# Performance work log

Measured on AMD Instinct MI355X. Metric: run time of the kernel, lower is better.

Reference implementation:

```python
import jax, jax.numpy as jnp
import numpy as np

B, PIX_H, PIX_W = 64, 14, 14
ENC_D, DEC_D, ATT_D, EMB_D = 2048, 512, 512, 512
VOCAB, MAX_LEN = 10000, 52  # 51 decode steps


def setup_inputs() -> dict:
    key = jax.random.key(0)
    ks = jax.random.split(key, 24)
    s = 0.02
    inp = {
        'encoder_out': jax.random.normal(ks[0], (B, PIX_H, PIX_W, ENC_D), jnp.float32),
        'encoded_captions': jax.random.randint(ks[1], (B, MAX_LEN), 0, VOCAB),
        'caption_lengths': jnp.sort(jax.random.randint(ks[2], (B,), 2, MAX_LEN + 1))[::-1].at[0].set(MAX_LEN),
        # embedding (uniform -0.1..0.1 as in init_weights)
        'emb': jax.random.uniform(ks[3], (VOCAB, EMB_D), jnp.float32, -0.1, 0.1),
        # attention network
        'W_enc_att': jax.random.normal(ks[4], (ENC_D, ATT_D)) * s,
        'b_enc_att': jnp.zeros((ATT_D,)),
        'W_dec_att': jax.random.normal(ks[5], (DEC_D, ATT_D)) * s,
        'b_dec_att': jnp.zeros((ATT_D,)),
        'W_full_att': jax.random.normal(ks[6], (ATT_D, 1)) * s,
        'b_full_att': jnp.zeros((1,)),
        # init hidden state
        'W_init_h': jax.random.normal(ks[7], (ENC_D, DEC_D)) * s,
        'b_init_h': jnp.zeros((DEC_D,)),
        'W_init_c': jax.random.normal(ks[8], (ENC_D, DEC_D)) * s,
        'b_init_c': jnp.zeros((DEC_D,)),
        # gate
        'W_fbeta': jax.random.normal(ks[9], (DEC_D, ENC_D)) * s,
        'b_fbeta': jnp.zeros((ENC_D,)),
        # LSTMCell (torch gate order i,f,g,o)
        'W_ih': jax.random.normal(ks[10], (EMB_D + ENC_D, 4 * DEC_D)) * s,
        'W_hh': jax.random.normal(ks[11], (DEC_D, 4 * DEC_D)) * s,
        'b_ih': jnp.zeros((4 * DEC_D,)),
        'b_hh': jnp.zeros((4 * DEC_D,)),
        # fc (uniform -0.1..0.1, zero bias per init_weights)
        'W_fc': jax.random.uniform(ks[12], (DEC_D, VOCAB), jnp.float32, -0.1, 0.1),
        'b_fc': jnp.zeros((VOCAB,)),
    }
    return inp


def _decode(encoder_out, encoded_captions, caption_lengths, emb,
            W_enc_att, b_enc_att, W_dec_att, b_dec_att, W_full_att, b_full_att,
            W_init_h, b_init_h, W_init_c, b_init_c, W_fbeta, b_fbeta,
            W_ih, W_hh, b_ih, b_hh, W_fc, b_fc):
    bsz = encoder_out.shape[0]
    enc = encoder_out.reshape(bsz, -1, encoder_out.shape[-1])  # [B, P, ENC_D]
    embeddings = emb[encoded_captions]                          # [B, T+1, E]
    mean_enc = enc.mean(axis=1)
    h0 = mean_enc @ W_init_h + b_init_h
    c0 = mean_enc @ W_init_c + b_init_c
    att_enc = enc @ W_enc_att + b_enc_att                       # [B, P, A] precomputed
    T = encoded_captions.shape[1] - 1                           # max decode steps
    decode_len = caption_lengths - 1                            # [B]
    step_mask = jnp.arange(T)[:, None] < decode_len[None, :]    # [T, B]
    emb_seq = jnp.swapaxes(embeddings[:, :T, :], 0, 1)          # [T, B, E]

    def step(carry, xt):
        h, c = carry
        emb_t, m = xt                                           # [B,E], [B]
        # attention: 2 linears + tanh + softmax + weighted sum
        att_dec = h @ W_dec_att + b_dec_att                     # [B, A]
        e = (jnp.tanh(att_enc + att_dec[:, None, :]) @ W_full_att + b_full_att)[..., 0]  # [B, P]
        alpha = jax.nn.softmax(e, axis=-1)
        awe = jnp.einsum('bp,bpd->bd', alpha, enc)              # [B, ENC_D]
        gate = jax.nn.sigmoid(h @ W_fbeta + b_fbeta)
        awe = gate * awe
        # LSTMCell
        x = jnp.concatenate([emb_t, awe], axis=1)
        gates = x @ W_ih + h @ W_hh + (b_ih + b_hh)
        i, f, g, o = jnp.split(gates, 4, axis=1)
        c_new = jax.nn.sigmoid(f) * c + jax.nn.sigmoid(i) * jnp.tanh(g)
        h_new = jax.nn.sigmoid(o) * jnp.tanh(c_new)
        mm = m[:, None]
        h = jnp.where(mm, h_new, h)  # freeze finished rows (== batch_size_t slicing)
        c = jnp.where(mm, c_new, c)
        preds = (h @ W_fc + b_fc) * mm  # dropout = identity (eval mode)
        return (h, c), (preds, alpha * mm)

    (_, _), (preds_seq, alpha_seq) = jax.lax.scan(step, (h0, c0), (emb_seq, step_mask))
    predictions = jnp.swapaxes(preds_seq, 0, 1)  # [B, T, V]
    alphas = jnp.swapaxes(alpha_seq, 0, 1)       # [B, T, P]
    return predictions, alphas


def reference(encoder_out, encoded_captions, caption_lengths, emb,
              W_enc_att, b_enc_att, W_dec_att, b_dec_att, W_full_att, b_full_att,
              W_init_h, b_init_h, W_init_c, b_init_c, W_fbeta, b_fbeta,
              W_ih, W_hh, b_ih, b_hh, W_fc, b_fc):
    predictions, alphas = _decode(encoder_out, encoded_captions, caption_lengths, emb,
                                  W_enc_att, b_enc_att, W_dec_att, b_dec_att, W_full_att, b_full_att,
                                  W_init_h, b_init_h, W_init_c, b_init_c, W_fbeta, b_fbeta,
                                  W_ih, W_hh, b_ih, b_hh, W_fc, b_fc)
    return predictions, encoded_captions, caption_lengths - 1, alphas
```

## Files before the change

### kernel.cpp

```cpp
#include <hip/hip_runtime.h>
#include <hip/hip_bf16.h>
#include <math.h>

#define BB 64
#define NPIX 196
#define ENCD 2048
#define DECD 512
#define VOCAB_N 10000
#define MAXLEN 52
#define TT 51
#define NOUT 12608

#define PRED_SZ   (BB * TT * VOCAB_N)
#define CAPS_SZ   (BB * MAXLEN)
#define LENS_SZ   (BB)
#define ALPHAS_OFF (PRED_SZ + CAPS_SZ + LENS_SZ)

typedef __attribute__((ext_vector_type(8))) short short8;
typedef __attribute__((ext_vector_type(4))) short short4v;
typedef __attribute__((ext_vector_type(4))) float f32x4;

__device__ __forceinline__ float fsigm(float x) {
    return 1.0f / (1.0f + __expf(-x));
}
__device__ __forceinline__ float ftanh(float x) {
    x = fminf(fmaxf(x, -15.0f), 15.0f);
    float e = __expf(2.0f * x);
    return (e - 1.0f) / (e + 1.0f);
}
__device__ __forceinline__ float bf2f(unsigned short u) {
    union { unsigned int i; float f; } v;
    v.i = ((unsigned int)u) << 16;
    return v.f;
}
__device__ __forceinline__ unsigned short f2bf(float f) {
    union { float f; unsigned int i; } v;
    v.f = f;
    unsigned int r = v.i + 0x7FFFu + ((v.i >> 16) & 1u);
    return (unsigned short)(r >> 16);
}

__global__ __launch_bounds__(256) void gemm_mfma(
    const unsigned short* __restrict__ A, int lda,
    const unsigned short* __restrict__ Wp, int Npad,
    int nkb, long slice_stride,
    float* __restrict__ C, unsigned short* __restrict__ C16, long ldc,
    const float* __restrict__ bias, int N, int act,
    const int* __restrict__ caplen, int t)
{
    const int n0 = blockIdx.x * 64;
    const int m0 = blockIdx.y * 64;
    const int kz = blockIdx.z;
    A  += (size_t)kz * nkb * 32;
    Wp += (size_t)kz * nkb * Npad * 32;
    if (C) C += (size_t)kz * slice_stride;

    const int w  = threadIdx.x >> 6;
    const int l  = threadIdx.x & 63;
    const int lr = l & 15;
    const int q  = l >> 4;

    const unsigned short* ap = A + (size_t)(m0 + 16 * w + lr) * lda + q * 8;
    const unsigned short* bp = Wp + (size_t)(n0 + lr) * 32 + q * 8;
    const size_t bstep = (size_t)Npad * 32;

    f32x4 acc[4];
#pragma unroll
    for (int i = 0; i < 4; ++i) acc[i] = (f32x4){0.f, 0.f, 0.f, 0.f};

    short8 a  = *(const short8*)ap;
    short8 b0 = *(const short8*)(bp);
    short8 b1 = *(const short8*)(bp + 512);
    short8 b2 = *(const short8*)(bp + 1024);
    short8 b3 = *(const short8*)(bp + 1536);

    for (int kb = 0; kb < nkb; ++kb) {
        const size_t nxt = (kb + 1 < nkb) ? 1 : 0;
        const unsigned short* apn = ap + nxt * 32;
        const unsigned short* bpn = bp + nxt * bstep;
        short8 an  = *(const short8*)apn;
        short8 bn0 = *(const short8*)(bpn);
        short8 bn1 = *(const short8*)(bpn + 512);
        short8 bn2 = *(const short8*)(bpn + 1024);
        short8 bn3 = *(const short8*)(bpn + 1536);
        acc[0] = __builtin_amdgcn_mfma_f32_16x16x32_bf16(a, b0, acc[0], 0, 0, 0);
        acc[1] = __builtin_amdgcn_mfma_f32_16x16x32_bf16(a, b1, acc[1], 0, 0, 0);
        acc[2] = __builtin_amdgcn_mfma_f32_16x16x32_bf16(a, b2, acc[2], 0, 0, 0);
        acc[3] = __builtin_amdgcn_mfma_f32_16x16x32_bf16(a, b3, acc[3], 0, 0, 0);
        a = an; b0 = bn0; b1 = bn1; b2 = bn2; b3 = bn3;
        ap = apn; bp = bpn;
    }

    const int r0 = q * 4;
#pragma unroll
    for (int cf = 0; cf < 4; ++cf) {
        int col = n0 + cf * 16 + lr;
        if (col >= N) continue;
        float bv = bias ? bias[col] : 0.f;
#pragma unroll
        for (int r = 0; r < 4; ++r) {
            int row = m0 + 16 * w + r0 + r;
            float v = acc[cf][r] + bv;
            if (act == 1 || (act == 2 && col < 2048)) v = fsigm(v);
            if (caplen) v *= (t < caplen[row] - 1) ? 1.f : 0.f;
            if (C16) C16[(size_t)row * ldc + col] = f2bf(v);
            else     C [(size_t)row * ldc + col] = v;
        }
    }
}

__global__ __launch_bounds__(256) void outgemm_kernel(
    const unsigned short* __restrict__ h16,
    const unsigned short* __restrict__ Wp,
    const float* __restrict__ bias,
    const int* __restrict__ caplen, int t,
    float* __restrict__ preds, long ldc,
    float* __restrict__ gadec, int nbase)
{
    const int n0 = (nbase + blockIdx.x) * 64;
    const int w  = threadIdx.x >> 6;
    const int l  = threadIdx.x & 63;
    const int lr = l & 15;
    const int q  = l >> 4;

    const unsigned short* ap = h16 + (size_t)(16 * w + lr) * 3072 + q * 8;
    const unsigned short* bp = Wp + (size_t)(n0 + lr) * 32 + q * 8;
    const size_t bstep = (size_t)NOUT * 32;

    f32x4 acc[4];
#pragma unroll
    for (int i = 0; i < 4; ++i) acc[i] = (f32x4){0.f, 0.f, 0.f, 0.f};

    short8 a  = *(const short8*)ap;
    short8 b0 = *(const short8*)(bp);
    short8 b1 = *(const short8*)(bp + 512);
    short8 b2 = *(const short8*)(bp + 1024);
    short8 b3 = *(const short8*)(bp + 1536);

    for (int kb = 0; kb < 16; ++kb) {
        const size_t nxt = (kb + 1 < 16) ? 1 : 0;
        const unsigned short* apn = ap + nxt * 32;
        const unsigned short* bpn = bp + nxt * bstep;
        short8 an  = *(const short8*)apn;
        short8 bn0 = *(const short8*)(bpn);
        short8 bn1 = *(const short8*)(bpn + 512);
        short8 bn2 = *(const short8*)(bpn + 1024);
        short8 bn3 = *(const short8*)(bpn + 1536);
        acc[0] = __builtin_amdgcn_mfma_f32_16x16x32_bf16(a, b0, acc[0], 0, 0, 0);
        acc[1] = __builtin_amdgcn_mfma_f32_16x16x32_bf16(a, b1, acc[1], 0, 0, 0);
        acc[2] = __builtin_amdgcn_mfma_f32_16x16x32_bf16(a, b2, acc[2], 0, 0, 0);
        acc[3] = __builtin_amdgcn_mfma_f32_16x16x32_bf16(a, b3, acc[3], 0, 0, 0);
        a = an; b0 = bn0; b1 = bn1; b2 = bn2; b3 = bn3;
        ap = apn; bp = bpn;
    }

    const int r0 = q * 4;
#pragma unroll
    for (int cf = 0; cf < 4; ++cf) {
        int col = n0 + cf * 16 + lr;
        float bv = bias[col];
#pragma unroll
        for (int r = 0; r < 4; ++r) {
            int row = 16 * w + r0 + r;
            float v = acc[cf][r] + bv;
            if (col < VOCAB_N) {
                float mk = (t < caplen[row] - 1) ? 1.f : 0.f;
                preds[(size_t)row * ldc + col] = v * mk;
            } else if (col < 10048) {
            } else if (col < 12096) {
                gadec[(size_t)row * 2560 + (col - 10048)] = fsigm(v);
            } else {
                gadec[(size_t)row * 2560 + 2048 + (col - 12096)] = v;
            }
        }
    }
}

__global__ void pack_kernel(const float* __restrict__ W1, const float* __restrict__ W2,
                            int N1, int N2, int K1, int Npad, int mode,
                            unsigned short* __restrict__ Wp, int total)
{
    int idx = blockIdx.x * 256 + threadIdx.x;
    if (idx >= total) return;
    int kk = idx & 31;
    int r  = idx >> 5;
    int n  = r % Npad;
    int kb = r / Npad;
    int k  = kb * 32 + kk;
    float v = 0.f;
    if (mode == 0) {
        if (n < N1) v = W1[(size_t)k * N1 + n];
    } else if (mode == 1) {
        v = (n < N1) ? W1[(size_t)k * N1 + n] : W2[(size_t)k * N2 + (n - N1)];
    } else {
        v = (k < K1) ? W1[(size_t)k * N1 + n] : W2[(size_t)(k - K1) * N1 + n];
    }
    Wp[idx] = f2bf(v);
}

__global__ void pack3_kernel(const float* __restrict__ Wfc,
                             const float* __restrict__ Wfb,
                             const float* __restrict__ Wda,
                             unsigned short* __restrict__ Wp, int total)
{
    int idx = blockIdx.x * 256 + threadIdx.x;
    if (idx >= total) return;
    int kk = idx & 31;
    int r  = idx >> 5;
    int n  = r % NOUT;
    int kb = r / NOUT;
    int k  = kb * 32 + kk;
    float v = 0.f;
    if (n < VOCAB_N)       v = Wfc[(size_t)k * VOCAB_N + n];
    else if (n < 10048)    v = 0.f;
    else if (n < 12096)    v = Wfb[(size_t)k * 2048 + (n - 10048)];
    else                   v = Wda[(size_t)k * 512 + (n - 12096)];
    Wp[idx] = f2bf(v);
}

__global__ void cast_kernel(const float* __restrict__ src,
                            unsigned short* __restrict__ dst, int n)
{
    int i = (blockIdx.x * 256 + threadIdx.x) * 4;
    if (i >= n) return;
    float4 v = *(const float4*)(src + i);
    dst[i]     = f2bf(v.x);
    dst[i + 1] = f2bf(v.y);
    dst[i + 2] = f2bf(v.z);
    dst[i + 3] = f2bf(v.w);
}

__global__ void bias_prep(const float* __restrict__ bfc, const float* __restrict__ bfb,
                          const float* __restrict__ bda, const float* __restrict__ bih,
                          const float* __restrict__ bhh,
                          float* __restrict__ bcat2, float* __restrict__ bsum)
{
    int i = blockIdx.x * 256 + threadIdx.x;
    if (i < VOCAB_N) bcat2[i] = bfc[i];
    else if (i < 10048) bcat2[i] = 0.f;
    else if (i < 12096) bcat2[i] = bfb[i - 10048];
    else if (i < NOUT) bcat2[i] = bda[i - 12096];
    else if (i < NOUT + 2048) { int j = i - NOUT; bsum[j] = bih[j] + bhh[j]; }
}

__global__ void mean_kernel(const float* __restrict__ enc, float* __restrict__ me)
{
    int d = blockIdx.x * 256 + threadIdx.x;
    int b = blockIdx.y;
    const float* p = enc + (size_t)b * NPIX * ENCD + d;
    float s = 0.0f;
    for (int q = 0; q < NPIX; ++q) s += p[(size_t)q * ENCD];
    me[b * ENCD + d] = s * (1.0f / 196.0f);
}

__global__ void inithc_kernel(const float* __restrict__ me,
                              const float* __restrict__ Wh, const float* __restrict__ bh,
                              const float* __restrict__ Wc, const float* __restrict__ bc,
                              unsigned short* __restrict__ xcat, float* __restrict__ c)
{
    int idx = blockIdx.x * 256 + threadIdx.x;
    int b = idx >> 9, j = idx & 511;
    const float* m = me + b * ENCD;
    float sh = bh[j], sc = bc[j];
    for (int k = 0; k < ENCD; ++k) {
        float mv = m[k];
        sh += mv * Wh[(size_t)k * DECD + j];
        sc += mv * Wc[(size_t)k * DECD + j];
    }
    xcat[(size_t)b * 3072 + 2560 + j] = f2bf(sh);
    c[idx] = sc;
}

__global__ void copy_misc(const int* __restrict__ caps, const int* __restrict__ lens,
                          float* __restrict__ out)
{
    int i = blockIdx.x * 256 + threadIdx.x;
    if (i < CAPS_SZ) out[PRED_SZ + i] = (float)caps[i];
    else if (i < CAPS_SZ + LENS_SZ) out[PRED_SZ + i] = (float)(lens[i - CAPS_SZ] - 1);
}

__global__ __launch_bounds__(512) void attawe_kernel(
    const float* __restrict__ gadec,
    const unsigned short* __restrict__ attenc16,
    const unsigned short* __restrict__ enc16,
    const float* __restrict__ Wf, const float* __restrict__ bf_,
    const float* __restrict__ emb, const int* __restrict__ caps,
    const int* __restrict__ caplen, int t,
    unsigned short* __restrict__ xcat,
    float* __restrict__ alphas_out)
{
    int b = blockIdx.x;
    int tid = threadIdx.x;
    int lane = tid & 63, wid = tid >> 6;
    __shared__ float av[512];
    __shared__ float wv[512];
    __shared__ float es[NPIX];
    __shared__ float alpha_s[NPIX];
    __shared__ float r8[8];
    __shared__ float smax, ssum;

    av[tid] = gadec[(size_t)b * 2560 + 2048 + tid];
    wv[tid] = Wf[tid];
    __syncthreads();

    float mya[8], myw[8];
#pragma unroll
    for (int i = 0; i < 8; ++i) {
        mya[i] = av[lane * 8 + i];
        myw[i] = wv[lane * 8 + i];
    }

    float bf0 = bf_[0];
    for (int p = wid; p < NPIX; p += 8) {
        const unsigned short* ae = attenc16 + ((size_t)(b * NPIX + p)) * 512 + lane * 8;
        short8 e8 = *(const short8*)ae;
        float s = 0.f;
#pragma unroll
        for (int i = 0; i < 8; ++i)
            s += ftanh(bf2f((unsigned short)e8[i]) + mya[i]) * myw[i];
        for (int off = 32; off; off >>= 1) s += __shfl_down(s, off);
        if (lane == 0) es[p] = s + bf0;
    }
    __syncthreads();

    float v = (tid < NPIX) ? es[tid] : -1e30f;
    float m = v;
    for (int off = 32; off; off >>= 1) m = fmaxf(m, __shfl_down(m, off));
    if (lane == 0) r8[wid] = m;
    __syncthreads();
    if (tid == 0) {
        float mm = r8[0];
#pragma unroll
        for (int i = 1; i < 8; ++i) mm = fmaxf(mm, r8[i]);
        smax = mm;
    }
    __syncthreads();

    float ev = (tid < NPIX) ? __expf(v - smax) : 0.0f;
    float s = ev;
    for (int off = 32; off; off >>= 1) s += __shfl_down(s, off);
    if (lane == 0) r8[wid] = s;
    __syncthreads();
    if (tid == 0) {
        float ss = 0.f;
#pragma unroll
        for (int i = 0; i < 8; ++i) ss += r8[i];
        ssum = ss;
    }
    __syncthreads();

    float mk = (t < caplen[b] - 1) ? 1.0f : 0.0f;
    if (tid < NPIX) {
        float a = ev / ssum;
        alpha_s[tid] = a;
        alphas_out[((size_t)b * TT + t) * NPIX + tid] = a * mk;
    }
    __syncthreads();

    int d0 = tid * 4;
    const unsigned short* e = enc16 + (size_t)b * NPIX * ENCD + d0;
    float s0 = 0.f, s1 = 0.f, s2 = 0.f, s3 = 0.f;
    for (int p = 0; p < NPIX; ++p) {
        short4v v4 = *(const short4v*)(e + (size_t)p * ENCD);
        float a = alpha_s[p];
        s0 += a * bf2f((unsigned short)v4[0]);
        s1 += a * bf2f((unsigned short)v4[1]);
        s2 += a * bf2f((unsigned short)v4[2]);
        s3 += a * bf2f((unsigned short)v4[3]);
    }
    unsigned short* xr = xcat + (size_t)b * 3072;
    const float* gt = gadec + (size_t)b * 2560 + d0;
    xr[512 + d0 + 0] = f2bf(s0 * gt[0]);
    xr[512 + d0 + 1] = f2bf(s1 * gt[1]);
    xr[512 + d0 + 2] = f2bf(s2 * gt[2]);
    xr[512 + d0 + 3] = f2bf(s3 * gt[3]);

    int wword = caps[b * MAXLEN + t];
    xr[tid] = f2bf(emb[(size_t)wword * 512 + tid]);
}

__global__ __launch_bounds__(256) void lstm_kernel(
    const float* __restrict__ gparts, const float* __restrict__ bsum,
    const int* __restrict__ caplen, int t,
    float* __restrict__ c, unsigned short* __restrict__ xcat)
{
    int idx = blockIdx.x * 256 + threadIdx.x;
    int b = idx >> 9, j = idx & 511;
    const float* g = gparts + (size_t)b * 2048;
    float gi = bsum[j],        gf = bsum[512 + j];
    float gg = bsum[1024 + j], go = bsum[1536 + j];
#pragma unroll
    for (int s = 0; s < 8; ++s) {
        const float* p = g + (size_t)s * BB * 2048;
        gi += p[j]; gf += p[512 + j]; gg += p[1024 + j]; go += p[1536 + j];
    }
    float cn = fsigm(gf) * c[idx] + fsigm(gi) * ftanh(gg);
    float hn = fsigm(go) * ftanh(cn);
    if (t < caplen[b] - 1) {
        c[idx] = cn;
        xcat[(size_t)b * 3072 + 2560 + j] = f2bf(hn);
    }
}

extern "C" void kernel_launch(void* const* d_in, const int* in_sizes, int n_in,
                              void* d_out, int out_size, void* d_ws, size_t ws_size,
                              hipStream_t stream)
{
    (void)in_sizes; (void)n_in; (void)out_size; (void)ws_size;
    const float* enc        = (const float*)d_in[0];
    const int*   caps       = (const int*)d_in[1];
    const int*   lens       = (const int*)d_in[2];
    const float* emb        = (const float*)d_in[3];
    const float* W_enc_att  = (const float*)d_in[4];
    const float* b_enc_att  = (const float*)d_in[5];
    const float* W_dec_att  = (const float*)d_in[6];
    const float* b_dec_att  = (const float*)d_in[7];
    const float* W_full_att = (const float*)d_in[8];
    const float* b_full_att = (const float*)d_in[9];
    const float* W_init_h   = (const float*)d_in[10];
    const float* b_init_h   = (const float*)d_in[11];
    const float* W_init_c   = (const float*)d_in[12];
    const float* b_init_c   = (const float*)d_in[13];
    const float* W_fbeta    = (const float*)d_in[14];
    const float* b_fbeta    = (const float*)d_in[15];
    const float* W_ih       = (const float*)d_in[16];
    const float* W_hh       = (const float*)d_in[17];
    const float* b_ih       = (const float*)d_in[18];
    const float* b_hh       = (const float*)d_in[19];
    const float* W_fc       = (const float*)d_in[20];
    const float* b_fc       = (const float*)d_in[21];
    float* out = (float*)d_out;

    char* p = (char*)d_ws;
    unsigned short* enc16   = (unsigned short*)p; p += (size_t)BB * NPIX * ENCD * 2;
    unsigned short* attenc16= (unsigned short*)p; p += (size_t)BB * NPIX * 512 * 2;
    unsigned short* WpL     = (unsigned short*)p; p += (size_t)96 * 2048 * 32 * 2;
    unsigned short* WpO     = (unsigned short*)p; p += (size_t)16 * NOUT * 32 * 2;
    unsigned short* WpE     = (unsigned short*)p; p += (size_t)64 * 512 * 32 * 2;
    unsigned short* xcat    = (unsigned short*)p; p += (size_t)BB * 3072 * 2;
    float* gadec  = (float*)p; p += (size_t)BB * 2560 * 4;
    float* gparts = (float*)p; p += (size_t)8 * BB * 2048 * 4;
    float* c      = (float*)p; p += (size_t)BB * 512 * 4;
    float* me     = (float*)p; p += (size_t)BB * ENCD * 4;
    float* bcat2  = (float*)p; p += NOUT * 4;
    float* bsum   = (float*)p; p += 2048 * 4;

    {
        int n = BB * NPIX * ENCD;
        cast_kernel<<<(n / 4 + 255) / 256, 256, 0, stream>>>(enc, enc16, n);
    }
    { int tot = 96 * 2048 * 32;
      pack_kernel<<<(tot + 255) / 256, 256, 0, stream>>>(W_ih, W_hh, 2048, 2048, 2560, 2048, 2, WpL, tot); }
    { int tot = 16 * NOUT * 32;
      pack3_kernel<<<(tot + 255) / 256, 256, 0, stream>>>(W_fc, W_fbeta, W_dec_att, WpO, tot); }
    { int tot = 64 * 512 * 32;
      pack_kernel<<<(tot + 255) / 256, 256, 0, stream>>>(W_enc_att, nullptr, 512, 0, 0, 512, 0, WpE, tot); }
    bias_prep<<<(NOUT + 2048 + 255) / 256, 256, 0, stream>>>(b_fc, b_fbeta, b_dec_att, b_ih, b_hh, bcat2, bsum);
    mean_kernel<<<dim3(8, 64), 256, 0, stream>>>(enc, me);
    inithc_kernel<<<128, 256, 0, stream>>>(me, W_init_h, b_init_h, W_init_c, b_init_c, xcat, c);
    gemm_mfma<<<dim3(8, 196, 1), 256, 0, stream>>>(
        enc16, ENCD, WpE, 512, 64, 0, nullptr, attenc16, 512,
        b_enc_att, 512, 0, nullptr, 0);
    copy_misc<<<14, 256, 0, stream>>>(caps, lens, out);

    const unsigned short* h16 = xcat + 2560;

    outgemm_kernel<<<40, 256, 0, stream>>>(
        h16, WpO, bcat2, lens, 0, out, (long)TT * VOCAB_N, gadec, 157);

    for (int t = 0; t < TT; ++t) {
        attawe_kernel<<<64, 512, 0, stream>>>(
            gadec, attenc16, enc16, W_full_att, b_full_att,
            emb, caps, lens, t, xcat, out + ALPHAS_OFF);
        gemm_mfma<<<dim3(32, 1, 8), 256, 0, stream>>>(
            xcat, 3072, WpL, 2048, 12, (long)BB * 2048, gparts, nullptr, 2048,
            nullptr, 2048, 0, nullptr, 0);
        lstm_kernel<<<128, 256, 0, stream>>>(gparts, bsum, lens, t, c, xcat);
        outgemm_kernel<<<197, 256, 0, stream>>>(
            h16, WpO, bcat2, lens, t, out + (size_t)t * VOCAB_N,
            (long)TT * VOCAB_N, gadec, 0);
    }
}
```

Before: 3.448 ms.

## Fuse decode loop into one persistent cooperative kernel with grid syncs

Replaces the per-timestep sequence of four kernel launches (attention, gates GEMM, LSTM, output GEMM) across 51 steps with one cooperative kernel of 256 blocks that loops over time and separates phases with grid-wide syncs. The attention phase now runs with 256 threads per block instead of 512, each thread handling 8 channels. The encoder-attention GEMM also moves to a larger 128x128 register-tiled kernel for more data reuse. The aim is to remove around two hundred launch overheads, at the cost of grid.sync latency and lower parallelism in the attention phase.

New measurement: 12.00 ms. 3.48x slower.

```diff
diff --git a/kernel.cpp b/kernel.cpp
--- a/kernel.cpp
+++ b/kernel.cpp
@@ -1,6 +1,9 @@
 #include <hip/hip_runtime.h>
 #include <hip/hip_bf16.h>
+#include <hip/hip_cooperative_groups.h>
 #include <math.h>
+
+namespace cg = cooperative_groups;
 
 #define BB 64
 #define NPIX 196
@@ -17,7 +20,6 @@
 #define ALPHAS_OFF (PRED_SZ + CAPS_SZ + LENS_SZ)
 
 typedef __attribute__((ext_vector_type(8))) short short8;
-typedef __attribute__((ext_vector_type(4))) short short4v;
 typedef __attribute__((ext_vector_type(4))) float f32x4;
 
 __device__ __forceinline__ float fsigm(float x) {
@@ -40,29 +42,128 @@
     return (unsigned short)(r >> 16);
 }
 
-__global__ __launch_bounds__(256) void gemm_mfma(
-    const unsigned short* __restrict__ A, int lda,
-    const unsigned short* __restrict__ Wp, int Npad,
-    int nkb, long slice_stride,
-    float* __restrict__ C, unsigned short* __restrict__ C16, long ldc,
-    const float* __restrict__ bias, int N, int act,
-    const int* __restrict__ caplen, int t)
-{
-    const int n0 = blockIdx.x * 64;
-    const int m0 = blockIdx.y * 64;
-    const int kz = blockIdx.z;
-    A  += (size_t)kz * nkb * 32;
-    Wp += (size_t)kz * nkb * Npad * 32;
-    if (C) C += (size_t)kz * slice_stride;
+struct DecP {
+    const unsigned short* attenc16;
+    const unsigned short* enc16;
+    unsigned short* xcat;
+    float* gadec;
+    float* gparts;
+    float* c;
+    const float* Wf;
+    const float* bfull;
+    const float* emb;
+    const int* caps;
+    const int* lens;
+    const unsigned short* WpL;
+    const unsigned short* WpO;
+    const float* bcat2;
+    const float* bsum;
+    float* out;
+};
+
+__device__ __forceinline__ void attawe_phase(const DecP& P, int t)
+{
+    __shared__ float av[512];
+    __shared__ float wv[512];
+    __shared__ float es[NPIX];
+    __shared__ float alpha_s[NPIX];
+    __shared__ float r4[4];
+    __shared__ float smax, ssum;
+
+    const int b = blockIdx.x;
+    const int tid = threadIdx.x;
+    const int lane = tid & 63, wid = tid >> 6;
+
+    for (int j = tid; j < 512; j += 256) {
+        av[j] = P.gadec[(size_t)b * 2560 + 2048 + j];
+        wv[j] = P.Wf[j];
+    }
+    __syncthreads();
+
+    float mya[8], myw[8];
+#pragma unroll
+    for (int i = 0; i < 8; ++i) {
+        mya[i] = av[lane * 8 + i];
+        myw[i] = wv[lane * 8 + i];
+    }
+
+    float bf0 = P.bfull[0];
+    for (int p = wid; p < NPIX; p += 4) {
+        const unsigned short* ae = P.attenc16 + ((size_t)(b * NPIX + p)) * 512 + lane * 8;
+        short8 e8 = *(const short8*)ae;
+        float s = 0.f;
+#pragma unroll
+        for (int i = 0; i < 8; ++i)
+            s += ftanh(bf2f((unsigned short)e8[i]) + mya[i]) * myw[i];
+        for (int off = 32; off; off >>= 1) s += __shfl_down(s, off);
+        if (lane == 0) es[p] = s + bf0;
+    }
+    __syncthreads();
+
+    float v = (tid < NPIX) ? es[tid] : -1e30f;
+    float m = v;
+    for (int off = 32; off; off >>= 1) m = fmaxf(m, __shfl_down(m, off));
+    if (lane == 0) r4[wid] = m;
+    __syncthreads();
+    if (tid == 0) smax = fmaxf(fmaxf(r4[0], r4[1]), fmaxf(r4[2], r4[3]));
+    __syncthreads();
+
+    float ev = (tid < NPIX) ? __expf(v - smax) : 0.0f;
+    float s = ev;
+    for (int off = 32; off; off >>= 1) s += __shfl_down(s, off);
+    if (lane == 0) r4[wid] = s;
+    __syncthreads();
+    if (tid == 0) ssum = r4[0] + r4[1] + r4[2] + r4[3];
+    __syncthreads();
+
+    float mk = (t < P.lens[b] - 1) ? 1.0f : 0.0f;
+    if (tid < NPIX) {
+        float a = ev / ssum;
+        alpha_s[tid] = a;
+        P.out[ALPHAS_OFF + ((size_t)b * TT + t) * NPIX + tid] = a * mk;
+    }
+    __syncthreads();
+
+    int d0 = tid * 8;
+    const unsigned short* e = P.enc16 + (size_t)b * NPIX * ENCD + d0;
+    float sa[8];
+#pragma unroll
+    for (int j = 0; j < 8; ++j) sa[j] = 0.f;
+#pragma unroll 4
+    for (int p = 0; p < NPIX; ++p) {
+        short8 v8 = *(const short8*)(e + (size_t)p * ENCD);
+        float a = alpha_s[p];
+#pragma unroll
+        for (int j = 0; j < 8; ++j) sa[j] += a * bf2f((unsigned short)v8[j]);
+    }
+    unsigned short* xr = P.xcat + (size_t)b * 3072;
+    const float* gt = P.gadec + (size_t)b * 2560 + d0;
+#pragma unroll
+    for (int j = 0; j < 8; ++j)
+        xr[512 + d0 + j] = f2bf(sa[j] * gt[j]);
+
+    int wword = P.caps[b * MAXLEN + t];
+    for (int j = tid; j < 512; j += 256)
+        xr[j] = f2bf(P.emb[(size_t)wword * 512 + j]);
+}
+
+__device__ __forceinline__ void gates_phase(const DecP& P)
+{
+    const int bx = blockIdx.x;
+    const int nx = bx & 31, kz = bx >> 5;
+    const int n0 = nx * 64;
+    const unsigned short* A  = P.xcat + kz * 384;
+    const unsigned short* Wp = P.WpL + (size_t)kz * 12 * 2048 * 32;
+    float* C = P.gparts + (size_t)kz * BB * 2048;
 
     const int w  = threadIdx.x >> 6;
     const int l  = threadIdx.x & 63;
     const int lr = l & 15;
     const int q  = l >> 4;
 
-    const unsigned short* ap = A + (size_t)(m0 + 16 * w + lr) * lda + q * 8;
+    const unsigned short* ap = A + (size_t)(16 * w + lr) * 3072 + q * 8;
     const unsigned short* bp = Wp + (size_t)(n0 + lr) * 32 + q * 8;
-    const size_t bstep = (size_t)Npad * 32;
+    const size_t bstep = (size_t)2048 * 32;
 
     f32x4 acc[4];
 #pragma unroll
@@ -74,8 +175,8 @@
     short8 b2 = *(const short8*)(bp + 1024);
     short8 b3 = *(const short8*)(bp + 1536);
 
-    for (int kb = 0; kb < nkb; ++kb) {
-        const size_t nxt = (kb + 1 < nkb) ? 1 : 0;
+    for (int kb = 0; kb < 12; ++kb) {
+        const size_t nxt = (kb + 1 < 12) ? 1 : 0;
         const unsigned short* apn = ap + nxt * 32;
         const unsigned short* bpn = bp + nxt * bstep;
         short8 an  = *(const short8*)apn;
@@ -95,36 +196,44 @@
 #pragma unroll
     for (int cf = 0; cf < 4; ++cf) {
         int col = n0 + cf * 16 + lr;
-        if (col >= N) continue;
-        float bv = bias ? bias[col] : 0.f;
 #pragma unroll
         for (int r = 0; r < 4; ++r) {
-            int row = m0 + 16 * w + r0 + r;
-            float v = acc[cf][r] + bv;
-            if (act == 1 || (act == 2 && col < 2048)) v = fsigm(v);
-            if (caplen) v *= (t < caplen[row] - 1) ? 1.f : 0.f;
-            if (C16) C16[(size_t)row * ldc + col] = f2bf(v);
-            else     C [(size_t)row * ldc + col] = v;
+            int row = 16 * w + r0 + r;
+            C[(size_t)row * 2048 + col] = acc[cf][r];
         }
     }
 }
 
-__global__ __launch_bounds__(256) void outgemm_kernel(
-    const unsigned short* __restrict__ h16,
-    const unsigned short* __restrict__ Wp,
-    const float* __restrict__ bias,
-    const int* __restrict__ caplen, int t,
-    float* __restrict__ preds, long ldc,
-    float* __restrict__ gadec, int nbase)
-{
-    const int n0 = (nbase + blockIdx.x) * 64;
+__device__ __forceinline__ void lstm_phase(const DecP& P, int t)
+{
+    int idx = blockIdx.x * 256 + threadIdx.x;
+    int b = idx >> 9, j = idx & 511;
+    const float* g = P.gparts + (size_t)b * 2048;
+    float gi = P.bsum[j],        gf = P.bsum[512 + j];
+    float gg = P.bsum[1024 + j], go = P.bsum[1536 + j];
+#pragma unroll
+    for (int s = 0; s < 8; ++s) {
+        const float* p = g + (size_t)s * BB * 2048;
+        gi += p[j]; gf += p[512 + j]; gg += p[1024 + j]; go += p[1536 + j];
+    }
+    float cn = fsigm(gf) * P.c[idx] + fsigm(gi) * ftanh(gg);
+    float hn = fsigm(go) * ftanh(cn);
+    if (t < P.lens[b] - 1) {
+        P.c[idx] = cn;
+        P.xcat[(size_t)b * 3072 + 2560 + j] = f2bf(hn);
+    }
+}
+
+__device__ __forceinline__ void outgemm_phase(const DecP& P, int t)
+{
+    const int n0 = blockIdx.x * 64;
     const int w  = threadIdx.x >> 6;
     const int l  = threadIdx.x & 63;
     const int lr = l & 15;
     const int q  = l >> 4;
 
-    const unsigned short* ap = h16 + (size_t)(16 * w + lr) * 3072 + q * 8;
-    const unsigned short* bp = Wp + (size_t)(n0 + lr) * 32 + q * 8;
+    const unsigned short* ap = P.xcat + 2560 + (size_t)(16 * w + lr) * 3072 + q * 8;
+    const unsigned short* bp = P.WpO + (size_t)(n0 + lr) * 32 + q * 8;
     const size_t bstep = (size_t)NOUT * 32;
 
     f32x4 acc[4];
@@ -154,23 +263,107 @@
         ap = apn; bp = bpn;
     }
 
+    float* preds = P.out + (size_t)t * VOCAB_N;
     const int r0 = q * 4;
 #pragma unroll
     for (int cf = 0; cf < 4; ++cf) {
         int col = n0 + cf * 16 + lr;
-        float bv = bias[col];
+        float bv = P.bcat2[col];
 #pragma unroll
         for (int r = 0; r < 4; ++r) {
             int row = 16 * w + r0 + r;
             float v = acc[cf][r] + bv;
             if (col < VOCAB_N) {
-                float mk = (t < caplen[row] - 1) ? 1.f : 0.f;
-                preds[(size_t)row * ldc + col] = v * mk;
+                float mk = (t < P.lens[row] - 1) ? 1.f : 0.f;
+                preds[(size_t)row * ((size_t)TT * VOCAB_N) + col] = v * mk;
             } else if (col < 10048) {
             } else if (col < 12096) {
-                gadec[(size_t)row * 2560 + (col - 10048)] = fsigm(v);
+                P.gadec[(size_t)row * 2560 + (col - 10048)] = fsigm(v);
             } else {
-                gadec[(size_t)row * 2560 + 2048 + (col - 12096)] = v;
+                P.gadec[(size_t)row * 2560 + 2048 + (col - 12096)] = v;
+            }
+        }
+    }
+}
+
+__global__ __launch_bounds__(256) void decode_loop(DecP P)
+{
+    cg::grid_group grid = cg::this_grid();
+    const int bx = blockIdx.x;
+
+    if (bx >= 157 && bx < 197) outgemm_phase(P, 0);
+    grid.sync();
+
+    for (int t = 0; t < TT; ++t) {
+        if (bx < 64) attawe_phase(P, t);
+        grid.sync();
+        gates_phase(P);
+        grid.sync();
+        if (bx < 128) lstm_phase(P, t);
+        grid.sync();
+        if (bx < 197) outgemm_phase(P, t);
+        grid.sync();
+    }
+}
+
+__global__ __launch_bounds__(256) void encatt_gemm(
+    const unsigned short* __restrict__ A,
+    const unsigned short* __restrict__ Wp,
+    const float* __restrict__ bias,
+    unsigned short* __restrict__ C16)
+{
+    const int n0 = blockIdx.x * 128;
+    const int m0 = blockIdx.y * 128;
+    const int w  = threadIdx.x >> 6;
+    const int l  = threadIdx.x & 63;
+    const int lr = l & 15;
+    const int q  = l >> 4;
+
+    const unsigned short* ap = A + (size_t)(m0 + 16 * w + lr) * 2048 + q * 8;
+    const unsigned short* bp = Wp + (size_t)(n0 + lr) * 32 + q * 8;
+    const size_t bstep = (size_t)512 * 32;
+
+    f32x4 acc[16];
+#pragma unroll
+    for (int i = 0; i < 16; ++i) acc[i] = (f32x4){0.f, 0.f, 0.f, 0.f};
+
+    short8 a0 = *(const short8*)(ap);
+    short8 a1 = *(const short8*)(ap + 64 * 2048);
+    short8 b[8];
+#pragma unroll
+    for (int nt = 0; nt < 8; ++nt) b[nt] = *(const short8*)(bp + nt * 512);
+
+    for (int kb = 0; kb < 64; ++kb) {
+        const size_t nxt = (kb + 1 < 64) ? 1 : 0;
+        const unsigned short* apn = ap + nxt * 32;
+        const unsigned short* bpn = bp + nxt * bstep;
+        short8 an0 = *(const short8*)(apn);
+        short8 an1 = *(const short8*)(apn + 64 * 2048);
+        short8 bn[8];
+#pragma unroll
+        for (int nt = 0; nt < 8; ++nt) bn[nt] = *(const short8*)(bpn + nt * 512);
+#pragma unroll
+        for (int nt = 0; nt < 8; ++nt) {
+            acc[nt]     = __builtin_amdgcn_mfma_f32_16x16x32_bf16(a0, b[nt], acc[nt], 0, 0, 0);
+            acc[8 + nt] = __builtin_amdgcn_mfma_f32_16x16x32_bf16(a1, b[nt], acc[8 + nt], 0, 0, 0);
+        }
+        a0 = an0; a1 = an1;
+#pragma unroll
+        for (int nt = 0; nt < 8; ++nt) b[nt] = bn[nt];
+        ap = apn; bp = bpn;
+    }
+
+    const int r0 = q * 4;
+#pragma unroll
+    for (int mt = 0; mt < 2; ++mt) {
+#pragma unroll
+        for (int nt = 0; nt < 8; ++nt) {
+            int col = n0 + nt * 16 + lr;
+            float bv = bias[col];
+#pragma unroll
+            for (int r = 0; r < 4; ++r) {
+                int row = m0 + mt * 64 + 16 * w + r0 + r;
+                C16[(size_t)row * 512 + col] = f2bf(acc[mt * 8 + nt][r] + bv);
             }
         }
     }
@@ -277,129 +470,6 @@
     int i = blockIdx.x * 256 + threadIdx.x;
     if (i < CAPS_SZ) out[PRED_SZ + i] = (float)caps[i];
     else if (i < CAPS_SZ + LENS_SZ) out[PRED_SZ + i] = (float)(lens[i - CAPS_SZ] - 1);
-}
-
-__global__ __launch_bounds__(512) void attawe_kernel(
-    const float* __restrict__ gadec,
-    const unsigned short* __restrict__ attenc16,
-    const unsigned short* __restrict__ enc16,
-    const float* __restrict__ Wf, const float* __restrict__ bf_,
-    const float* __restrict__ emb, const int* __restrict__ caps,
-    const int* __restrict__ caplen, int t,
-    unsigned short* __restrict__ xcat,
-    float* __restrict__ alphas_out)
-{
-    int b = blockIdx.x;
-    int tid = threadIdx.x;
-    int lane = tid & 63, wid = tid >> 6;
-    __shared__ float av[512];
-    __shared__ float wv[512];
-    __shared__ float es[NPIX];
-    __shared__ float alpha_s[NPIX];
-    __shared__ float r8[8];
-    __shared__ float smax, ssum;
-
-    av[tid] = gadec[(size_t)b * 2560 + 2048 + tid];
-    wv[tid] = Wf[tid];
-    __syncthreads();
-
-    float mya[8], myw[8];
-#pragma unroll
-    for (int i = 0; i < 8; ++i) {
-        mya[i] = av[lane * 8 + i];
-        myw[i] = wv[lane * 8 + i];
-    }
-
-    float bf0 = bf_[0];
-    for (int p = wid; p < NPIX; p += 8) {
-        const unsigned short* ae = attenc16 + ((size_t)(b * NPIX + p)) * 512 + lane * 8;
-        short8 e8 = *(const short8*)ae;
-        float s = 0.f;
-#pragma unroll
-        for (int i = 0; i < 8; ++i)
-            s += ftanh(bf2f((unsigned short)e8[i]) + mya[i]) * myw[i];
-        for (int off = 32; off; off >>= 1) s += __shfl_down(s, off);
-        if (lane == 0) es[p] = s + bf0;
-    }
-    __syncthreads();
-
-    float v = (tid < NPIX) ? es[tid] : -1e30f;
-    float m = v;
-    for (int off = 32; off; off >>= 1) m = fmaxf(m, __shfl_down(m, off));
-    if (lane == 0) r8[wid] = m;
-    __syncthreads();
-    if (tid == 0) {
-        float mm = r8[0];
-#pragma unroll
-        for (int i = 1; i < 8; ++i) mm = fmaxf(mm, r8[i]);
-        smax = mm;
-    }
-    __syncthreads();
-
-    float ev = (tid < NPIX) ? __expf(v - smax) : 0.0f;
-    float s = ev;
-    for (int off = 32; off; off >>= 1) s += __shfl_down(s, off);
-    if (lane == 0) r8[wid] = s;
-    __syncthreads();
-    if (tid == 0) {
-        float ss = 0.f;
-#pragma unroll
-        for (int i = 0; i < 8; ++i) ss += r8[i];
-        ssum = ss;
-    }
-    __syncthreads();
-
-    float mk = (t < caplen[b] - 1) ? 1.0f : 0.0f;
-    if (tid < NPIX) {
-        float a = ev / ssum;
-        alpha_s[tid] = a;
-        alphas_out[((size_t)b * TT + t) * NPIX + tid] = a * mk;
-    }
-    __syncthreads();
-
-    int d0 = tid * 4;
-    const unsigned short* e = enc16 + (size_t)b * NPIX * ENCD + d0;
-    float s0 = 0.f, s1 = 0.f, s2 = 0.f, s3 = 0.f;
-    for (int p = 0; p < NPIX; ++p) {
-        short4v v4 = *(const short4v*)(e + (size_t)p * ENCD);
-        float a = alpha_s[p];
-        s0 += a * bf2f((unsigned short)v4[0]);
-        s1 += a * bf2f((unsigned short)v4[1]);
-        s2 += a * bf2f((unsigned short)v4[2]);
-        s3 += a * bf2f((unsigned short)v4[3]);
-    }
-    unsigned short* xr = xcat + (size_t)b * 3072;
-    const float* gt = gadec + (size_t)b * 2560 + d0;
-    xr[512 + d0 + 0] = f2bf(s0 * gt[0]);
-    xr[512 + d0 + 1] = f2bf(s1 * gt[1]);
-    xr[512 + d0 + 2] = f2bf(s2 * gt[2]);
-    xr[512 + d0 + 3] = f2bf(s3 * gt[3]);
-
-    int wword = caps[b * MAXLEN + t];
-    xr[tid] = f2bf(emb[(size_t)wword * 512 + tid]);
-}
-
-__global__ __launch_bounds__(256) void lstm_kernel(
-    const float* __restrict__ gparts, const float* __restrict__ bsum,
-    const int* __restrict__ caplen, int t,
-    float* __restrict__ c, unsigned short* __restrict__ xcat)
-{
-    int idx = blockIdx.x * 256 + threadIdx.x;
-    int b = idx >> 9, j = idx & 511;
-    const float* g = gparts + (size_t)b * 2048;
-    float gi = bsum[j],        gf = bsum[512 + j];
-    float gg = bsum[1024 + j], go = bsum[1536 + j];
-#pragma unroll
-    for (int s = 0; s < 8; ++s) {
-        const float* p = g + (size_t)s * BB * 2048;
-        gi += p[j]; gf += p[512 + j]; gg += p[1024 + j]; go += p[1536 + j];
-    }
-    float cn = fsigm(gf) * c[idx] + fsigm(gi) * ftanh(gg);
-    float hn = fsigm(go) * ftanh(cn);
-    if (t < caplen[b] - 1) {
-        c[idx] = cn;
-        xcat[(size_t)b * 3072 + 2560 + j] = f2bf(hn);
-    }
 }
 
 extern "C" void kernel_launch(void* const* d_in, const int* in_sizes, int n_in,
@@ -458,26 +528,28 @@
     bias_prep<<<(NOUT + 2048 + 255) / 256, 256, 0, stream>>>(b_fc, b_fbeta, b_dec_att, b_ih, b_hh, bcat2, bsum);
     mean_kernel<<<dim3(8, 64), 256, 0, stream>>>(enc, me);
     inithc_kernel<<<128, 256, 0, stream>>>(me, W_init_h, b_init_h, W_init_c, b_init_c, xcat, c);
-    gemm_mfma<<<dim3(8, 196, 1), 256, 0, stream>>>(
-        enc16, ENCD, WpE, 512, 64, 0, nullptr, attenc16, 512,
-        b_enc_att, 512, 0, nullptr, 0);
+    encatt_gemm<<<dim3(4, 98), 256, 0, stream>>>(enc16, WpE, b_enc_att, attenc16);
     copy_misc<<<14, 256, 0, stream>>>(caps, lens, out);
 
-    const unsigned short* h16 = xcat + 2560;
-
-    outgemm_kernel<<<40, 256, 0, stream>>>(
-        h16, WpO, bcat2, lens, 0, out, (long)TT * VOCAB_N, gadec, 157);
-
-    for (int t = 0; t < TT; ++t) {
-        attawe_kernel<<<64, 512, 0, stream>>>(
-            gadec, attenc16, enc16, W_full_att, b_full_att,
-            emb, caps, lens, t, xcat, out + ALPHAS_OFF);
-        gemm_mfma<<<dim3(32, 1, 8), 256, 0, stream>>>(
-            xcat, 3072, WpL, 2048, 12, (long)BB * 2048, gparts, nullptr, 2048,
-            nullptr, 2048, 0, nullptr, 0);
-        lstm_kernel<<<128, 256, 0, stream>>>(gparts, bsum, lens, t, c, xcat);
-        outgemm_kernel<<<197, 256, 0, stream>>>(
-            h16, WpO, bcat2, lens, t, out + (size_t)t * VOCAB_N,
-            (long)TT * VOCAB_N, gadec, 0);
-    }
-}
+    DecP P;
+    P.attenc16 = attenc16;
+    P.enc16    = enc16;
+    P.xcat     = xcat;
+    P.gadec    = gadec;
+    P.gparts   = gparts;
+    P.c        = c;
+    P.Wf       = W_full_att;
+    P.bfull    = b_full_att;
+    P.emb      = emb;
+    P.caps     = caps;
+    P.lens     = lens;
+    P.WpL      = WpL;
+    P.WpO      = WpO;
+    P.bcat2    = bcat2;
+    P.bsum     = bsum;
+    P.out      = out;
+
+    void* args[] = { &P };
+    hipLaunchCooperativeKernel(reinterpret_cast<void*>(decode_loop),
+                               dim3(256), dim3(256), args, 0, stream);
+}
```

## Defer vocab projection to one batched GEMM and fuse gate GEMM with LSTM

Applied to the files above, without the earlier changes.

The vocabulary projection (h @ W_fc) is taken out of the per-step loop. Each step now records h into a history buffer, and one large GEMM over all 51 steps writes the masked predictions at the end. The gate GEMM and the LSTM pointwise update are fused into one kernel: gate columns are interleaved so a block owns all four gates for its units, and a two-way K split is reduced in shared memory, replacing the 8-way split-K partials buffer. The per-step recurrent work shrinks to the small fbeta/dec_att projection, and the encoder attention GEMM gets a larger dedicated tile kernel. In exchange the fused gate kernel runs on only 32 blocks, which may limit parallelism on the serial critical path.

Measured after the change: 5.034 ms. 46.0% more time.

```diff
diff --git a/kernel.cpp b/kernel.cpp
--- a/kernel.cpp
+++ b/kernel.cpp
@@ -9,7 +9,7 @@
 #define VOCAB_N 10000
 #define MAXLEN 52
 #define TT 51
-#define NOUT 12608
+#define NPADFC 10048
 
 #define PRED_SZ   (BB * TT * VOCAB_N)
 #define CAPS_SZ   (BB * MAXLEN)
@@ -17,7 +17,6 @@
 #define ALPHAS_OFF (PRED_SZ + CAPS_SZ + LENS_SZ)
 
 typedef __attribute__((ext_vector_type(8))) short short8;
-typedef __attribute__((ext_vector_type(4))) short short4v;
 typedef __attribute__((ext_vector_type(4))) float f32x4;
 
 __device__ __forceinline__ float fsigm(float x) {
@@ -109,23 +108,108 @@
     }
 }
 
-__global__ __launch_bounds__(256) void outgemm_kernel(
-    const unsigned short* __restrict__ h16,
-    const unsigned short* __restrict__ Wp,
-    const float* __restrict__ bias,
+__global__ __launch_bounds__(512) void gates_lstm_kernel(
+    unsigned short* __restrict__ xcat,
+    const unsigned short* __restrict__ WpLi,
+    const float* __restrict__ bsum,
     const int* __restrict__ caplen, int t,
-    float* __restrict__ preds, long ldc,
-    float* __restrict__ gadec, int nbase)
-{
-    const int n0 = (nbase + blockIdx.x) * 64;
+    float* __restrict__ c,
+    unsigned short* __restrict__ hhist)
+{
+    __shared__ float gt[2][64][68];
+
+    const int n0 = blockIdx.x * 64;
+    const int j0 = blockIdx.x * 16;
+    const int tid = threadIdx.x;
+    const int ws = tid >> 8;
+    const int w  = (tid >> 6) & 3;
+    const int l  = tid & 63;
+    const int lr = l & 15;
+    const int q  = l >> 4;
+
+    const unsigned short* A  = xcat + ws * 1536;
+    const unsigned short* Wp = WpLi + (size_t)ws * 48 * 2048 * 32;
+
+    const unsigned short* ap = A + (size_t)(16 * w + lr) * 3072 + q * 8;
+    const unsigned short* bp = Wp + (size_t)(n0 + lr) * 32 + q * 8;
+    const size_t bstep = (size_t)2048 * 32;
+
+    f32x4 acc[4];
+#pragma unroll
+    for (int i = 0; i < 4; ++i) acc[i] = (f32x4){0.f, 0.f, 0.f, 0.f};
+
+    short8 a  = *(const short8*)ap;
+    short8 b0 = *(const short8*)(bp);
+    short8 b1 = *(const short8*)(bp + 512);
+    short8 b2 = *(const short8*)(bp + 1024);
+    short8 b3 = *(const short8*)(bp + 1536);
+
+    for (int kb = 0; kb < 48; ++kb) {
+        const size_t nxt = (kb + 1 < 48) ? 1 : 0;
+        const unsigned short* apn = ap + nxt * 32;
+        const unsigned short* bpn = bp + nxt * bstep;
+        short8 an  = *(const short8*)apn;
+        short8 bn0 = *(const short8*)(bpn);
+        short8 bn1 = *(const short8*)(bpn + 512);
+        short8 bn2 = *(const short8*)(bpn + 1024);
+        short8 bn3 = *(const short8*)(bpn + 1536);
+        acc[0] = __builtin_amdgcn_mfma_f32_16x16x32_bf16(a, b0, acc[0], 0, 0, 0);
+        acc[1] = __builtin_amdgcn_mfma_f32_16x16x32_bf16(a, b1, acc[1], 0, 0, 0);
+        acc[2] = __builtin_amdgcn_mfma_f32_16x16x32_bf16(a, b2, acc[2], 0, 0, 0);
+        acc[3] = __builtin_amdgcn_mfma_f32_16x16x32_bf16(a, b3, acc[3], 0, 0, 0);
+        a = an; b0 = bn0; b1 = bn1; b2 = bn2; b3 = bn3;
+        ap = apn; bp = bpn;
+    }
+
+    const int r0 = q * 4;
+#pragma unroll
+    for (int cf = 0; cf < 4; ++cf) {
+#pragma unroll
+        for (int r = 0; r < 4; ++r)
+            gt[ws][16 * w + r0 + r][cf * 16 + lr] = acc[cf][r];
+    }
+    __syncthreads();
+
+#pragma unroll
+    for (int it = 0; it < 2; ++it) {
+        int item = tid + 512 * it;
+        int row = item & 63;
+        int jj  = item >> 6;
+        int j   = j0 + jj;
+        int lc  = 4 * jj;
+        float gi = gt[0][row][lc + 0] + gt[1][row][lc + 0] + bsum[j];
+        float gf = gt[0][row][lc + 1] + gt[1][row][lc + 1] + bsum[512 + j];
+        float gg = gt[0][row][lc + 2] + gt[1][row][lc + 2] + bsum[1024 + j];
+        float go = gt[0][row][lc + 3] + gt[1][row][lc + 3] + bsum[1536 + j];
+        int cidx = row * 512 + j;
+        float cn = fsigm(gf) * c[cidx] + fsigm(gi) * ftanh(gg);
+        float hn = fsigm(go) * ftanh(cn);
+        unsigned short* hx = xcat + (size_t)row * 3072 + 2560 + j;
+        unsigned short oldh = *hx;
+        bool upd = (t < caplen[row] - 1);
+        unsigned short hv = upd ? f2bf(hn) : oldh;
+        if (upd) { c[cidx] = cn; *hx = hv; }
+        hhist[((size_t)t * BB + row) * 512 + j] = hv;
+    }
+}
+
+__global__ __launch_bounds__(256) void preds_gemm(
+    const unsigned short* __restrict__ hhist,
+    const unsigned short* __restrict__ WpF,
+    const float* __restrict__ bfc,
+    const int* __restrict__ caplen,
+    float* __restrict__ out)
+{
+    const int n0 = blockIdx.x * 64;
+    const int row0 = blockIdx.y * 64;
     const int w  = threadIdx.x >> 6;
     const int l  = threadIdx.x & 63;
     const int lr = l & 15;
     const int q  = l >> 4;
 
-    const unsigned short* ap = h16 + (size_t)(16 * w + lr) * 3072 + q * 8;
-    const unsigned short* bp = Wp + (size_t)(n0 + lr) * 32 + q * 8;
-    const size_t bstep = (size_t)NOUT * 32;
+    const unsigned short* ap = hhist + (size_t)(row0 + 16 * w + lr) * 512 + q * 8;
+    const unsigned short* bp = WpF + (size_t)(n0 + lr) * 32 + q * 8;
+    const size_t bstep = (size_t)NPADFC * 32;
 
     f32x4 acc[4];
 #pragma unroll
@@ -158,20 +242,14 @@
 #pragma unroll
     for (int cf = 0; cf < 4; ++cf) {
         int col = n0 + cf * 16 + lr;
-        float bv = bias[col];
+        if (col >= VOCAB_N) continue;
+        float bv = bfc[col];
 #pragma unroll
         for (int r = 0; r < 4; ++r) {
-            int row = 16 * w + r0 + r;
-            float v = acc[cf][r] + bv;
-            if (col < VOCAB_N) {
-                float mk = (t < caplen[row] - 1) ? 1.f : 0.f;
-                preds[(size_t)row * ldc + col] = v * mk;
-            } else if (col < 10048) {
-            } else if (col < 12096) {
-                gadec[(size_t)row * 2560 + (col - 10048)] = fsigm(v);
-            } else {
-                gadec[(size_t)row * 2560 + 2048 + (col - 12096)] = v;
-            }
+            int row = row0 + 16 * w + r0 + r;
+            int tt = row >> 6, b = row & 63;
+            float mk = (tt < caplen[b] - 1) ? 1.f : 0.f;
+            out[((size_t)b * TT + tt) * VOCAB_N + col] = (acc[cf][r] + bv) * mk;
         }
     }
 }
@@ -198,23 +276,20 @@
     Wp[idx] = f2bf(v);
 }
 
-__global__ void pack3_kernel(const float* __restrict__ Wfc,
-                             const float* __restrict__ Wfb,
-                             const float* __restrict__ Wda,
-                             unsigned short* __restrict__ Wp, int total)
+__global__ void packGi_kernel(const float* __restrict__ Wih,
+                              const float* __restrict__ Whh,
+                              unsigned short* __restrict__ Wp, int total)
 {
     int idx = blockIdx.x * 256 + threadIdx.x;
     if (idx >= total) return;
     int kk = idx & 31;
     int r  = idx >> 5;
-    int n  = r % NOUT;
-    int kb = r / NOUT;
+    int n  = r % 2048;
+    int kb = r / 2048;
     int k  = kb * 32 + kk;
-    float v = 0.f;
-    if (n < VOCAB_N)       v = Wfc[(size_t)k * VOCAB_N + n];
-    else if (n < 10048)    v = 0.f;
-    else if (n < 12096)    v = Wfb[(size_t)k * 2048 + (n - 10048)];
-    else                   v = Wda[(size_t)k * 512 + (n - 12096)];
+    int oc = (n & 3) * 512 + (n >> 2);
+    float v = (k < 2560) ? Wih[(size_t)k * 2048 + oc]
+                         : Whh[(size_t)(k - 2560) * 2048 + oc];
     Wp[idx] = f2bf(v);
 }
 
@@ -230,17 +305,14 @@
     dst[i + 3] = f2bf(v.w);
 }
 
-__global__ void bias_prep(const float* __restrict__ bfc, const float* __restrict__ bfb,
-                          const float* __restrict__ bda, const float* __restrict__ bih,
-                          const float* __restrict__ bhh,
-                          float* __restrict__ bcat2, float* __restrict__ bsum)
+__global__ void bias_prep(const float* __restrict__ bfb, const float* __restrict__ bda,
+                          const float* __restrict__ bih, const float* __restrict__ bhh,
+                          float* __restrict__ bcat, float* __restrict__ bsum)
 {
     int i = blockIdx.x * 256 + threadIdx.x;
-    if (i < VOCAB_N) bcat2[i] = bfc[i];
-    else if (i < 10048) bcat2[i] = 0.f;
-    else if (i < 12096) bcat2[i] = bfb[i - 10048];
-    else if (i < NOUT) bcat2[i] = bda[i - 12096];
-    else if (i < NOUT + 2048) { int j = i - NOUT; bsum[j] = bih[j] + bhh[j]; }
+    if (i < 2048) bcat[i] = bfb[i];
+    else if (i < 2560) bcat[i] = bda[i - 2048];
+    else if (i < 2560 + 2048) { int j = i - 2560; bsum[j] = bih[j] + bhh[j]; }
 }
 
 __global__ void mean_kernel(const float* __restrict__ enc, float* __restrict__ me)
@@ -360,6 +432,7 @@
     int d0 = tid * 4;
     const unsigned short* e = enc16 + (size_t)b * NPIX * ENCD + d0;
     float s0 = 0.f, s1 = 0.f, s2 = 0.f, s3 = 0.f;
+    typedef __attribute__((ext_vector_type(4))) short short4v;
     for (int p = 0; p < NPIX; ++p) {
         short4v v4 = *(const short4v*)(e + (size_t)p * ENCD);
         float a = alpha_s[p];
@@ -379,26 +452,66 @@
     xr[tid] = f2bf(emb[(size_t)wword * 512 + tid]);
 }
 
-__global__ __launch_bounds__(256) void lstm_kernel(
-    const float* __restrict__ gparts, const float* __restrict__ bsum,
-    const int* __restrict__ caplen, int t,
-    float* __restrict__ c, unsigned short* __restrict__ xcat)
-{
-    int idx = blockIdx.x * 256 + threadIdx.x;
-    int b = idx >> 9, j = idx & 511;
-    const float* g = gparts + (size_t)b * 2048;
-    float gi = bsum[j],        gf = bsum[512 + j];
-    float gg = bsum[1024 + j], go = bsum[1536 + j];
-#pragma unroll
-    for (int s = 0; s < 8; ++s) {
-        const float* p = g + (size_t)s * BB * 2048;
-        gi += p[j]; gf += p[512 + j]; gg += p[1024 + j]; go += p[1536 + j];
-    }
-    float cn = fsigm(gf) * c[idx] + fsigm(gi) * ftanh(gg);
-    float hn = fsigm(go) * ftanh(cn);
-    if (t < caplen[b] - 1) {
-        c[idx] = cn;
-        xcat[(size_t)b * 3072 + 2560 + j] = f2bf(hn);
+__global__ __launch_bounds__(256) void encatt_gemm(
+    const unsigned short* __restrict__ A,
+    const unsigned short* __restrict__ Wp,
+    const float* __restrict__ bias,
+    unsigned short* __restrict__ C16)
+{
+    const int n0 = blockIdx.x * 128;
+    const int m0 = blockIdx.y * 128;
+    const int w  = threadIdx.x >> 6;
+    const int l  = threadIdx.x & 63;
+    const int lr = l & 15;
+    const int q  = l >> 4;
+
+    const unsigned short* ap = A + (size_t)(m0 + 16 * w + lr) * 2048 + q * 8;
+    const unsigned short* bp = Wp + (size_t)(n0 + lr) * 32 + q * 8;
+    const size_t bstep = (size_t)512 * 32;
+
+    f32x4 acc[16];
+#pragma unroll
+    for (int i = 0; i < 16; ++i) acc[i] = (f32x4){0.f, 0.f, 0.f, 0.f};
+
+    short8 a0 = *(const short8*)(ap);
+    short8 a1 = *(const short8*)(ap + 64 * 2048);
+    short8 b[8];
+#pragma unroll
+    for (int nt = 0; nt < 8; ++nt) b[nt] = *(const short8*)(bp + nt * 512);
+
+    for (int kb = 0; kb < 64; ++kb) {
+        const size_t nxt = (kb + 1 < 64) ? 1 : 0;
+        const unsigned short* apn = ap + nxt * 32;
+        const unsigned short* bpn = bp + nxt * bstep;
+        short8 an0 = *(const short8*)(apn);
+        short8 an1 = *(const short8*)(apn + 64 * 2048);
+        short8 bn[8];
+#pragma unroll
+        for (int nt = 0; nt < 8; ++nt) bn[nt] = *(const short8*)(bpn + nt * 512);
+#pragma unroll
+        for (int nt = 0; nt < 8; ++nt) {
+            acc[nt]     = __builtin_amdgcn_mfma_f32_16x16x32_bf16(a0, b[nt], acc[nt], 0, 0, 0);
+            acc[8 + nt] = __builtin_amdgcn_mfma_f32_16x16x32_bf16(a1, b[nt], acc[8 + nt], 0, 0, 0);
+        }
+        a0 = an0; a1 = an1;
+#pragma unroll
+        for (int nt = 0; nt < 8; ++nt) b[nt] = bn[nt];
+        ap = apn; bp = bpn;
+    }
+
+    const int r0 = q * 4;
+#pragma unroll
+    for (int mt = 0; mt < 2; ++mt) {
+#pragma unroll
+        for (int nt = 0; nt < 8; ++nt) {
+            int col = n0 + nt * 16 + lr;
+            float bv = bias[col];
+#pragma unroll
+            for (int r = 0; r < 4; ++r) {
+                int row = m0 + mt * 64 + 16 * w + r0 + r;
+                C16[(size_t)row * 512 + col] = f2bf(acc[mt * 8 + nt][r] + bv);
+            }
+        }
     }
 }
 
@@ -434,15 +547,16 @@
     char* p = (char*)d_ws;
     unsigned short* enc16   = (unsigned short*)p; p += (size_t)BB * NPIX * ENCD * 2;
     unsigned short* attenc16= (unsigned short*)p; p += (size_t)BB * NPIX * 512 * 2;
-    unsigned short* WpL     = (unsigned short*)p; p += (size_t)96 * 2048 * 32 * 2;
-    unsigned short* WpO     = (unsigned short*)p; p += (size_t)16 * NOUT * 32 * 2;
+    unsigned short* WpLi    = (unsigned short*)p; p += (size_t)96 * 2048 * 32 * 2;
+    unsigned short* WpG     = (unsigned short*)p; p += (size_t)16 * 2560 * 32 * 2;
+    unsigned short* WpF     = (unsigned short*)p; p += (size_t)16 * NPADFC * 32 * 2;
     unsigned short* WpE     = (unsigned short*)p; p += (size_t)64 * 512 * 32 * 2;
     unsigned short* xcat    = (unsigned short*)p; p += (size_t)BB * 3072 * 2;
+    unsigned short* hhist   = (unsigned short*)p; p += (size_t)TT * BB * 512 * 2;
     float* gadec  = (float*)p; p += (size_t)BB * 2560 * 4;
-    float* gparts = (float*)p; p += (size_t)8 * BB * 2048 * 4;
     float* c      = (float*)p; p += (size_t)BB * 512 * 4;
     float* me     = (float*)p; p += (size_t)BB * ENCD * 4;
-    float* bcat2  = (float*)p; p += NOUT * 4;
+    float* bcat   = (float*)p; p += 2560 * 4;
     float* bsum   = (float*)p; p += 2048 * 4;
 
     {
@@ -450,34 +564,35 @@
         cast_kernel<<<(n / 4 + 255) / 256, 256, 0, stream>>>(enc, enc16, n);
     }
     { int tot = 96 * 2048 * 32;
-      pack_kernel<<<(tot + 255) / 256, 256, 0, stream>>>(W_ih, W_hh, 2048, 2048, 2560, 2048, 2, WpL, tot); }
-    { int tot = 16 * NOUT * 32;
-      pack3_kernel<<<(tot + 255) / 256, 256, 0, stream>>>(W_fc, W_fbeta, W_dec_att, WpO, tot); }
+      packGi_kernel<<<(tot + 255) / 256, 256, 0, stream>>>(W_ih, W_hh, WpLi, tot); }
+    { int tot = 16 * 2560 * 32;
+      pack_kernel<<<(tot + 255) / 256, 256, 0, stream>>>(W_fbeta, W_dec_att, 2048, 512, 0, 2560, 1, WpG, tot); }
+    { int tot = 16 * NPADFC * 32;
+      pack_kernel<<<(tot + 255) / 256, 256, 0, stream>>>(W_fc, nullptr, VOCAB_N, 0, 0, NPADFC, 0, WpF, tot); }
     { int tot = 64 * 512 * 32;
       pack_kernel<<<(tot + 255) / 256, 256, 0, stream>>>(W_enc_att, nullptr, 512, 0, 0, 512, 0, WpE, tot); }
-    bias_prep<<<(NOUT + 2048 + 255) / 256, 256, 0, stream>>>(b_fc, b_fbeta, b_dec_att, b_ih, b_hh, bcat2, bsum);
+    bias_prep<<<18, 256, 0, stream>>>(b_fbeta, b_dec_att, b_ih, b_hh, bcat, bsum);
     mean_kernel<<<dim3(8, 64), 256, 0, stream>>>(enc, me);
     inithc_kernel<<<128, 256, 0, stream>>>(me, W_init_h, b_init_h, W_init_c, b_init_c, xcat, c);
-    gemm_mfma<<<dim3(8, 196, 1), 256, 0, stream>>>(
-        enc16, ENCD, WpE, 512, 64, 0, nullptr, attenc16, 512,
-        b_enc_att, 512, 0, nullptr, 0);
+    encatt_gemm<<<dim3(4, 98), 256, 0, stream>>>(enc16, WpE, b_enc_att, attenc16);
     copy_misc<<<14, 256, 0, stream>>>(caps, lens, out);
 
     const unsigned short* h16 = xcat + 2560;
 
-    outgemm_kernel<<<40, 256, 0, stream>>>(
-        h16, WpO, bcat2, lens, 0, out, (long)TT * VOCAB_N, gadec, 157);
+    gemm_mfma<<<dim3(40, 1, 1), 256, 0, stream>>>(
+        h16, 3072, WpG, 2560, 16, 0, gadec, nullptr, 2560,
+        bcat, 2560, 2, nullptr, 0);
 
     for (int t = 0; t < TT; ++t) {
         attawe_kernel<<<64, 512, 0, stream>>>(
             gadec, attenc16, enc16, W_full_att, b_full_att,
             emb, caps, lens, t, xcat, out + ALPHAS_OFF);
-        gemm_mfma<<<dim3(32, 1, 8), 256, 0, stream>>>(
-            xcat, 3072, WpL, 2048, 12, (long)BB * 2048, gparts, nullptr, 2048,
-            nullptr, 2048, 0, nullptr, 0);
-        lstm_kernel<<<128, 256, 0, stream>>>(gparts, bsum, lens, t, c, xcat);
-        outgemm_kernel<<<197, 256, 0, stream>>>(
-            h16, WpO, bcat2, lens, t, out + (size_t)t * VOCAB_N,
-            (long)TT * VOCAB_N, gadec, 0);
-    }
-}
+        gates_lstm_kernel<<<32, 512, 0, stream>>>(
+            xcat, WpLi, bsum, lens, t, c, hhist);
+        gemm_mfma<<<dim3(40, 1, 1), 256, 0, stream>>>(
+            h16, 3072, WpG, 2560, 16, 0, gadec, nullptr, 2560,
+            bcat, 2560, 2, nullptr, 0);
+    }
+
+    preds_gemm<<<dim3(157, TT), 256, 0, stream>>>(hhist, WpF, b_fc, lens, out);
+}
```
